# Kernel optimization log

Hardware: AMD Instinct MI355X
Metric: run time of the kernel (lower is better)

The kernel has to match this reference:

```python
import jax, jax.numpy as jnp
import numpy as np

NUM_NODES = 100000
NUM_EDGES = 2500000
NUM_GRAPHS = 512
NODE_DIM = 7
STATE_DIM = 32
M = 2
ROUNDS = 4


def setup_inputs() -> dict:
    key = jax.random.key(0)
    ks = jax.random.split(key, 16)
    x = jax.random.normal(ks[0], (NUM_NODES, NODE_DIM), dtype=jnp.float32)
    edge_index = jax.random.randint(ks[1], (2, NUM_EDGES), 0, NUM_NODES)
    batch = jnp.sort(jax.random.randint(ks[2], (NUM_NODES,), 0, NUM_GRAPHS))
    s = 1.0 / np.sqrt(STATE_DIM)
    W_in = jax.random.normal(ks[3], (NODE_DIM, STATE_DIM), dtype=jnp.float32) / np.sqrt(NODE_DIM)
    b_in = jnp.zeros((STATE_DIM,), dtype=jnp.float32)
    W_msg = jax.random.normal(ks[4], (ROUNDS, STATE_DIM, STATE_DIM), dtype=jnp.float32) * s
    b_msg = jnp.zeros((ROUNDS, STATE_DIM), dtype=jnp.float32)
    W_upd = jax.random.normal(ks[5], (ROUNDS, STATE_DIM, STATE_DIM), dtype=jnp.float32) * s
    b_upd = jnp.zeros((ROUNDS, STATE_DIM), dtype=jnp.float32)
    W_out = jax.random.normal(ks[6], (STATE_DIM, 2 * M), dtype=jnp.float32) * s
    b_out = jnp.zeros((2 * M,), dtype=jnp.float32)
    return {"x": x, "edge_index": edge_index, "batch": batch,
            "W_in": W_in, "b_in": b_in, "W_msg": W_msg, "b_msg": b_msg,
            "W_upd": W_upd, "b_upd": b_upd, "W_out": W_out, "b_out": b_out}


def reference(x, edge_index, batch, W_in, b_in, W_msg, b_msg, W_upd, b_upd, W_out, b_out):
    # input net
    state = jax.nn.relu(x @ W_in + b_in)  # (N, S)
    src, dst = edge_index[0], edge_index[1]
    for r in range(ROUNDS):
        message = jax.nn.relu(state @ W_msg[r] + b_msg[r])          # (N, S)
        gathered = message[src]                                      # (E, S) irregular gather
        aggregated = jax.ops.segment_sum(gathered, dst, num_segments=NUM_NODES)  # scatter-add
        state = state + jax.nn.relu(aggregated @ W_upd[r] + b_upd[r])
    graph_state = jax.ops.segment_sum(state, batch, num_segments=NUM_GRAPHS)     # (G, S)
    out = graph_state @ W_out + b_out                                # (G, 2M)
    mean, log_std = jnp.split(out, 2, axis=-1)
    # Gaussian head: return mean and std (scale = exp(log_std)) concatenated
    return jnp.concatenate([mean, jnp.exp(log_std)], axis=-1)
```

## Files before the change

### kernel.cpp

```cpp
#include <hip/hip_runtime.h>
#include <hip/hip_fp8.h>
#include <math.h>

#define N_NODES 100000
#define N_EDGES 2500000
#define N_GRAPHS 512
#define NODE_DIM 7
#define S 32
#define ROUNDS 4

#define BKT_SHIFT 7
#define BKT_NODES 128
#define NBKT ((N_NODES + BKT_NODES - 1) / BKT_NODES)
#define CAP 3712
#define NSLOT 64
#define SLOT_PAD 32

#define GN (N_NODES * S / 256)
#define GG (N_NODES / 16)

__device__ __forceinline__ void block_max_publish(float v, float* slots, int bid, int tid) {
    __shared__ float wmax[4];
#pragma unroll
    for (int o = 32; o > 0; o >>= 1) v = fmaxf(v, __shfl_xor(v, o, 64));
    if ((tid & 63) == 0) wmax[tid >> 6] = v;
    __syncthreads();
    if (tid == 0) {
        float m = fmaxf(fmaxf(wmax[0], wmax[1]), fmaxf(wmax[2], wmax[3]));
        atomicMax((unsigned int*)&slots[(bid & (NSLOT - 1)) * SLOT_PAD], __float_as_uint(m));
    }
}

__device__ __forceinline__ void acc4_fp8(unsigned int u, float& a0, float& a1,
                                         float& a2, float& a3) {
#if __has_builtin(__builtin_amdgcn_cvt_pk_f32_fp8)
    typedef float v2f __attribute__((ext_vector_type(2)));
    v2f lo = __builtin_amdgcn_cvt_pk_f32_fp8((int)u, false);
    v2f hi = __builtin_amdgcn_cvt_pk_f32_fp8((int)u, true);
    a0 += lo.x; a1 += lo.y; a2 += hi.x; a3 += hi.y;
#else
    __hip_fp8_e4m3 t0, t1, t2, t3;
    t0.__x = u & 0xff; t1.__x = (u >> 8) & 0xff;
    t2.__x = (u >> 16) & 0xff; t3.__x = (u >> 24) & 0xff;
    a0 += (float)t0; a1 += (float)t1; a2 += (float)t2; a3 += (float)t3;
#endif
}

__global__ void k_input(const float* __restrict__ x, const float* __restrict__ W_in,
                        const float* __restrict__ b_in, float* __restrict__ state,
                        float* __restrict__ graph_state, int* __restrict__ cursor,
                        float* __restrict__ tmpmax) {
    __shared__ float sW[NODE_DIM * S];
    __shared__ float sb[S];
    __shared__ float wmax[4];
    int tid = threadIdx.x;
    if (tid < NODE_DIM * S) sW[tid] = W_in[tid];
    if (tid < S) sb[tid] = b_in[tid];
    __syncthreads();
    int gid = blockIdx.x * blockDim.x + tid;
    if (gid < N_GRAPHS * S) graph_state[gid] = 0.f;
    if (gid < NBKT) cursor[gid] = 0;
    int n = gid >> 5, j = gid & 31;
    float acc = sb[j];
#pragma unroll
    for (int k = 0; k < NODE_DIM; k++) acc += x[n * NODE_DIM + k] * sW[k * S + j];
    float v = fmaxf(acc, 0.f);
    state[gid] = v;
#pragma unroll
    for (int o = 32; o > 0; o >>= 1) v = fmaxf(v, __shfl_xor(v, o, 64));
    if ((tid & 63) == 0) wmax[tid >> 6] = v;
    __syncthreads();
    if (tid == 0)
        tmpmax[blockIdx.x] = fmaxf(fmaxf(wmax[0], wmax[1]), fmaxf(wmax[2], wmax[3]));
}

__global__ void k_bin(const int* __restrict__ src, const int* __restrict__ dst,
                      int* __restrict__ cursor, int* __restrict__ binned,
                      const float* __restrict__ tmpmax, float* __restrict__ smax0) {
    __shared__ int cnt[NBKT];
    __shared__ int base[NBKT];
    __shared__ float red[16];
    int tid = threadIdx.x;
    if (blockIdx.x == 0) {
        float m = 0.f;
        for (int i = tid; i < GN; i += 1024) m = fmaxf(m, tmpmax[i]);
#pragma unroll
        for (int o = 32; o > 0; o >>= 1) m = fmaxf(m, __shfl_xor(m, o, 64));
        if ((tid & 63) == 0) red[tid >> 6] = m;
        __syncthreads();
        if (tid == 0) {
            float g = 0.f;
#pragma unroll
            for (int k = 0; k < 16; k++) g = fmaxf(g, red[k]);
            smax0[0] = g;
        } else if (tid < NSLOT) {
            smax0[tid * SLOT_PAD] = 0.f;
        }
    }
    int tile = (N_EDGES + gridDim.x - 1) / gridDim.x;
    int b0 = blockIdx.x * tile;
    int b1 = min(b0 + tile, N_EDGES);
    for (int i = tid; i < NBKT; i += blockDim.x) cnt[i] = 0;
    __syncthreads();
    int dv[10];
#pragma unroll
    for (int q = 0; q < 10; q++) {
        int e = b0 + tid + q * 1024;
        dv[q] = (e < b1) ? dst[e] : -1;
        if (dv[q] >= 0) atomicAdd(&cnt[dv[q] >> BKT_SHIFT], 1);
    }
    __syncthreads();
    for (int i = tid; i < NBKT; i += blockDim.x) {
        int c = cnt[i];
        base[i] = c ? atomicAdd(&cursor[i], c) : 0;
        cnt[i] = 0;
    }
    __syncthreads();
#pragma unroll
    for (int q = 0; q < 10; q++) {
        int e = b0 + tid + q * 1024;
        int d = dv[q];
        if (d >= 0) {
            int k = d >> BKT_SHIFT;
            int lpos = base[k] + atomicAdd(&cnt[k], 1);
            if (lpos < CAP)
                binned[(size_t)k * CAP + lpos] = (src[e] << BKT_SHIFT) | (d & (BKT_NODES - 1));
        }
    }
}

__global__ void k_fill2(const int* __restrict__ cursor, int* __restrict__ binned,
                        int* __restrict__ row_beg, int* __restrict__ row_end) {
    __shared__ int stage[CAP];
    __shared__ int cnt[BKT_NODES];
    __shared__ int sm[BKT_NODES];
    int tid = threadIdx.x;
    int bkt = blockIdx.x;
    int beg = bkt * CAP;
    int m = min(cursor[bkt], CAP);
    for (int i = tid; i < m; i += 256) stage[i] = binned[beg + i];
    if (tid < BKT_NODES) cnt[tid] = 0;
    __syncthreads();
    for (int i = tid; i < m; i += 256) atomicAdd(&cnt[stage[i] & (BKT_NODES - 1)], 1);
    __syncthreads();
    int v = 0;
    if (tid < BKT_NODES) { v = cnt[tid]; sm[tid] = v; }
    __syncthreads();
    for (int off = 1; off < BKT_NODES; off <<= 1) {
        int add = 0;
        if (tid < BKT_NODES && tid >= off) add = sm[tid - off];
        __syncthreads();
        if (tid < BKT_NODES) sm[tid] += add;
        __syncthreads();
    }
    if (tid < BKT_NODES) {
        int excl = sm[tid] - v;
        cnt[tid] = excl;
        int n = bkt * BKT_NODES + tid;
        if (n < N_NODES) { row_beg[n] = beg + excl; row_end[n] = beg + excl + v; }
    }
    __syncthreads();
    for (int i = tid; i < m; i += 256) {
        int ent = stage[i];
        int p = atomicAdd(&cnt[ent & (BKT_NODES - 1)], 1);
        binned[beg + p] = ent >> BKT_SHIFT;
    }
}

__global__ void k_msg(const float* __restrict__ state, const float* __restrict__ W,
                      const float* __restrict__ b, const float* __restrict__ smax_slots,
                      float* __restrict__ smax_next, float* __restrict__ inv_scale_out,
                      __hip_fp8_e4m3* __restrict__ message) {
    __shared__ float sW[S * S];
    __shared__ float sb[S];
    __shared__ float ssc[S];
    int tid = threadIdx.x;
    if (blockIdx.x < NSLOT && tid == 0) smax_next[blockIdx.x * SLOT_PAD] = 0.f;
    for (int i = tid; i < S * S; i += 256) sW[i] = W[i];
    if (tid < S) sb[tid] = b[tid];
    __syncthreads();
    if (tid < S) {
        float smax = 0.f;
#pragma unroll
        for (int k = 0; k < NSLOT; k++) smax = fmaxf(smax, smax_slots[k * SLOT_PAD]);
        float cs = 0.f;
#pragma unroll
        for (int k = 0; k < S; k++) cs += fabsf(sW[k * S + tid]);
        float bound = smax * cs + fabsf(sb[tid]) + 1e-20f;
        int e = (int)floorf(log2f(400.f / bound));
        e = max(-60, min(60, e));
        ssc[tid] = exp2f((float)e);
        if (blockIdx.x == 0) inv_scale_out[tid] = exp2f((float)-e);
    }
    __syncthreads();
    int gid = blockIdx.x * 256 + tid;
    int j = tid & 31;
    float my = state[gid];
    float acc = sb[j];
#pragma unroll
    for (int k = 0; k < S; k++) acc += __shfl(my, k, 32) * sW[k * S + j];
    float m = fminf(fmaxf(acc, 0.f) * ssc[j], 440.f);
    message[gid] = __hip_fp8_e4m3(m);
}

__global__ void k_gather_upd(const int* __restrict__ row_beg, const int* __restrict__ row_end,
                             const int* __restrict__ csr_src,
                             const unsigned char* __restrict__ message,
                             const float* __restrict__ W, const float* __restrict__ b,
                             const float* __restrict__ inv_scale,
                             float* __restrict__ state, float* __restrict__ smax_next) {
    __shared__ float sW[S * S];
    __shared__ float sb[S];
    __shared__ float si[S];
    int tid = threadIdx.x;
    for (int i = tid; i < S * S; i += 256) sW[i] = W[i];
    if (tid < S) { sb[tid] = b[tid]; si[tid] = inv_scale[tid]; }
    __syncthreads();
    int g = tid >> 5, j = tid & 31;
    int n0 = blockIdx.x * 16 + g * 2;
    int n1 = n0 + 1;
    int es = j >> 3;
    int qd = j & 7;
    int b0 = row_beg[n0], e0 = row_end[n0];
    int b1 = row_beg[n1], e1 = row_end[n1];
    float a0 = 0.f, a1 = 0.f, a2 = 0.f, a3 = 0.f;
    float c0 = 0.f, c1 = 0.f, c2 = 0.f, c3 = 0.f;
    int sid0 = (b0 + j < e0) ? csr_src[b0 + j] : 0;
    int sid1 = (b1 + j < e1) ? csr_src[b1 + j] : 0;
    while (b0 < e0 || b1 < e1) {
        unsigned int u0[8], u1[8];
#pragma unroll
        for (int p = 0; p < 8; p++) {
            int s = __shfl(sid0, p * 4 + es, 32);
            unsigned int* ap = (unsigned int*)(message + (unsigned)s * 32u + (unsigned)qd * 4u);
            u0[p] = __hip_atomic_load(ap, __ATOMIC_RELAXED, __HIP_MEMORY_SCOPE_AGENT);
        }
#pragma unroll
        for (int p = 0; p < 8; p++) {
            int s = __shfl(sid1, p * 4 + es, 32);
            unsigned int* ap = (unsigned int*)(message + (unsigned)s * 32u + (unsigned)qd * 4u);
            u1[p] = __hip_atomic_load(ap, __ATOMIC_RELAXED, __HIP_MEMORY_SCOPE_AGENT);
        }
        int nb0 = b0 + 32, nb1 = b1 + 32;
        int nsid0 = (nb0 + j < e0) ? csr_src[nb0 + j] : 0;
        int nsid1 = (nb1 + j < e1) ? csr_src[nb1 + j] : 0;
#pragma unroll
        for (int p = 0; p < 8; p++) {
            unsigned int uv = (b0 + p * 4 + es < e0) ? u0[p] : 0u;
            acc4_fp8(uv, a0, a1, a2, a3);
        }
#pragma unroll
        for (int p = 0; p < 8; p++) {
            unsigned int uv = (b1 + p * 4 + es < e1) ? u1[p] : 0u;
            acc4_fp8(uv, c0, c1, c2, c3);
        }
        b0 = nb0; b1 = nb1; sid0 = nsid0; sid1 = nsid1;
    }
    a0 += __shfl_xor(a0, 8, 32); a0 += __shfl_xor(a0, 16, 32);
    a1 += __shfl_xor(a1, 8, 32); a1 += __shfl_xor(a1, 16, 32);
    a2 += __shfl_xor(a2, 8, 32); a2 += __shfl_xor(a2, 16, 32);
    a3 += __shfl_xor(a3, 8, 32); a3 += __shfl_xor(a3, 16, 32);
    c0 += __shfl_xor(c0, 8, 32); c0 += __shfl_xor(c0, 16, 32);
    c1 += __shfl_xor(c1, 8, 32); c1 += __shfl_xor(c1, 16, 32);
    c2 += __shfl_xor(c2, 8, 32); c2 += __shfl_xor(c2, 16, 32);
    c3 += __shfl_xor(c3, 8, 32); c3 += __shfl_xor(c3, 16, 32);
    float s0 = si[4 * qd + 0], s1 = si[4 * qd + 1];
    float s2 = si[4 * qd + 2], s3 = si[4 * qd + 3];
    a0 *= s0; a1 *= s1; a2 *= s2; a3 *= s3;
    c0 *= s0; c1 *= s1; c2 *= s2; c3 *= s3;
    float u0v = sb[j], u1v = sb[j];
#pragma unroll
    for (int k = 0; k < S; k++) {
        float av, cv;
        switch (k & 3) {
            case 0: av = __shfl(a0, k >> 2, 32); cv = __shfl(c0, k >> 2, 32); break;
            case 1: av = __shfl(a1, k >> 2, 32); cv = __shfl(c1, k >> 2, 32); break;
            case 2: av = __shfl(a2, k >> 2, 32); cv = __shfl(c2, k >> 2, 32); break;
            default: av = __shfl(a3, k >> 2, 32); cv = __shfl(c3, k >> 2, 32); break;
        }
        float w = sW[k * S + j];
        u0v += av * w;
        u1v += cv * w;
    }
    size_t i0 = (size_t)n0 * S + j, i1 = (size_t)n1 * S + j;
    float ns0 = state[i0] + fmaxf(u0v, 0.f);
    float ns1 = state[i1] + fmaxf(u1v, 0.f);
    state[i0] = ns0;
    state[i1] = ns1;
    block_max_publish(fmaxf(ns0, ns1), smax_next, blockIdx.x, tid);
}

__global__ void k_pool(const float* __restrict__ state, const int* __restrict__ batch,
                       float* __restrict__ graph_state) {
    const int CHUNK = 32;
    const int nchunks = (N_NODES + CHUNK - 1) / CHUNK;
    int gid = blockIdx.x * blockDim.x + threadIdx.x;
    if (gid >= nchunks * S) return;
    int c = gid >> 5, j = gid & 31;
    int n0 = c * CHUNK;
    int n1 = min(n0 + CHUNK, N_NODES);
    float acc = 0.f;
    int curb = batch[n0];
    for (int n = n0; n < n1; n++) {
        int bn = batch[n];
        if (bn != curb) {
            atomicAdd(&graph_state[curb * S + j], acc);
            acc = 0.f;
            curb = bn;
        }
        acc += state[(size_t)n * S + j];
    }
    atomicAdd(&graph_state[curb * S + j], acc);
}

__global__ void k_head(const float* __restrict__ graph_state, const float* __restrict__ W_out,
                       const float* __restrict__ b_out, float* __restrict__ out) {
    int gid = blockIdx.x * blockDim.x + threadIdx.x;
    if (gid >= N_GRAPHS * 4) return;
    int g = gid >> 2, j = gid & 3;
    float acc = b_out[j];
#pragma unroll
    for (int k = 0; k < S; k++) acc += graph_state[g * S + k] * W_out[k * 4 + j];
    out[gid] = (j < 2) ? acc : expf(fminf(acc, 88.0f));
}

extern "C" void kernel_launch(void* const* d_in, const int* in_sizes, int n_in,
                              void* d_out, int out_size, void* d_ws, size_t ws_size,
                              hipStream_t stream) {
    const float* x     = (const float*)d_in[0];
    const int*   ei    = (const int*)d_in[1];
    const int*   batch = (const int*)d_in[2];
    const float* W_in  = (const float*)d_in[3];
    const float* b_in  = (const float*)d_in[4];
    const float* W_msg = (const float*)d_in[5];
    const float* b_msg = (const float*)d_in[6];
    const float* W_upd = (const float*)d_in[7];
    const float* b_upd = (const float*)d_in[8];
    const float* W_out = (const float*)d_in[9];
    const float* b_out = (const float*)d_in[10];
    float* out = (float*)d_out;

    float* state            = (float*)d_ws;
    __hip_fp8_e4m3* message = (__hip_fp8_e4m3*)(state + (size_t)N_NODES * S);
    float* graph_state      = (float*)((char*)message + (size_t)N_NODES * S);
    float* smax             = graph_state + N_GRAPHS * S;
    float* inv_scale        = smax + (ROUNDS + 1) * NSLOT * SLOT_PAD;
    float* tmpmax           = inv_scale + S;
    int*   row_beg          = (int*)(tmpmax + GN);
    int*   row_end          = row_beg + N_NODES;
    int*   cursor           = row_end + N_NODES;
    int*   binned           = cursor + NBKT;

    const int* src = ei;
    const int* dst = ei + N_EDGES;

    k_input<<<GN, dim3(256), 0, stream>>>(x, W_in, b_in, state, graph_state, cursor, tmpmax);
    k_bin<<<256, dim3(1024), 0, stream>>>(src, dst, cursor, binned, tmpmax, smax);
    k_fill2<<<NBKT, dim3(256), 0, stream>>>(cursor, binned, row_beg, row_end);

    for (int r = 0; r < ROUNDS; r++) {
        k_msg<<<GN, dim3(256), 0, stream>>>(state, W_msg + r * S * S, b_msg + r * S,
                                            smax + r * NSLOT * SLOT_PAD,
                                            smax + (r + 1) * NSLOT * SLOT_PAD,
                                            inv_scale, message);
        k_gather_upd<<<GG, dim3(256), 0, stream>>>(row_beg, row_end, binned,
                                                   (const unsigned char*)message,
                                                   W_upd + r * S * S, b_upd + r * S,
                                                   inv_scale, state,
                                                   smax + (r + 1) * NSLOT * SLOT_PAD);
    }

    const int CHUNK = 32;
    int nchunks = (N_NODES + CHUNK - 1) / CHUNK;
    int gP = (nchunks * S + 255) / 256;
    k_pool<<<gP, dim3(256), 0, stream>>>(state, batch, graph_state);

    k_head<<<(N_GRAPHS * 4 + 255) / 256, dim3(256), 0, stream>>>(graph_state, W_out, b_out, out);
}
```

Baseline: 369.9 us.

## Fuse CSR fill with first message kernel and enlarge dst buckets

Merges the bucket-local CSR fill and the round-0 message computation into one launch, where extra blocks beyond the bucket count run the message body, so one kernel launch goes away and the two independent jobs overlap. Buckets grow to 256 nodes with a larger capacity, which halves the bucket count and lets every thread of the 256-thread block own one node in the scan. The binning loop switches from a register-cached unrolled pass to a strided loop that reads dst twice. The gather kernel also drops software prefetching of the next csr_src chunk. Larger shared staging per block and the lost prefetch may cut occupancy and latency hiding.

```diff
diff --git a/kernel.cpp b/kernel.cpp
--- a/kernel.cpp
+++ b/kernel.cpp
@@ -9,10 +9,10 @@
 #define S 32
 #define ROUNDS 4
 
-#define BKT_SHIFT 7
-#define BKT_NODES 128
+#define BKT_SHIFT 8
+#define BKT_NODES 256
 #define NBKT ((N_NODES + BKT_NODES - 1) / BKT_NODES)
-#define CAP 3712
+#define CAP 7168
 #define NSLOT 64
 #define SLOT_PAD 32
 
@@ -46,6 +46,43 @@
 #endif
 }
 
+__device__ __forceinline__ void msg_body(int mb, int tid,
+                                         const float* __restrict__ state,
+                                         const float* __restrict__ W,
+                                         const float* __restrict__ b,
+                                         const float* __restrict__ smax_slots,
+                                         float* __restrict__ smax_next,
+                                         float* __restrict__ inv_scale_out,
+                                         __hip_fp8_e4m3* __restrict__ message,
+                                         float* sW, float* sb, float* ssc) {
+    if (mb < NSLOT && tid == 0) smax_next[mb * SLOT_PAD] = 0.f;
+    for (int i = tid; i < S * S; i += 256) sW[i] = W[i];
+    if (tid < S) sb[tid] = b[tid];
+    __syncthreads();
+    if (tid < S) {
+        float smax = 0.f;
+#pragma unroll
+        for (int k = 0; k < NSLOT; k++) smax = fmaxf(smax, smax_slots[k * SLOT_PAD]);
+        float cs = 0.f;
+#pragma unroll
+        for (int k = 0; k < S; k++) cs += fabsf(sW[k * S + tid]);
+        float bound = smax * cs + fabsf(sb[tid]) + 1e-20f;
+        int e = (int)floorf(log2f(400.f / bound));
+        e = max(-60, min(60, e));
+        ssc[tid] = exp2f((float)e);
+        if (mb == 0) inv_scale_out[tid] = exp2f((float)-e);
+    }
+    __syncthreads();
+    int gid = mb * 256 + tid;
+    int j = tid & 31;
+    float my = state[gid];
+    float acc = sb[j];
+#pragma unroll
+    for (int k = 0; k < S; k++) acc += __shfl(my, k, 32) * sW[k * S + j];
+    float m = fminf(fmaxf(acc, 0.f) * ssc[j], 440.f);
+    message[gid] = __hip_fp8_e4m3(m);
+}
+
 __global__ void k_input(const float* __restrict__ x, const float* __restrict__ W_in,
                         const float* __restrict__ b_in, float* __restrict__ state,
                         float* __restrict__ graph_state, int* __restrict__ cursor,
@@ -102,13 +139,8 @@
     int b1 = min(b0 + tile, N_EDGES);
     for (int i = tid; i < NBKT; i += blockDim.x) cnt[i] = 0;
     __syncthreads();
-    int dv[10];
-#pragma unroll
-    for (int q = 0; q < 10; q++) {
-        int e = b0 + tid + q * 1024;
-        dv[q] = (e < b1) ? dst[e] : -1;
-        if (dv[q] >= 0) atomicAdd(&cnt[dv[q] >> BKT_SHIFT], 1);
-    }
+    for (int e = b0 + tid; e < b1; e += blockDim.x)
+        atomicAdd(&cnt[dst[e] >> BKT_SHIFT], 1);
     __syncthreads();
     for (int i = tid; i < NBKT; i += blockDim.x) {
         int c = cnt[i];
@@ -116,53 +148,58 @@
         cnt[i] = 0;
     }
     __syncthreads();
-#pragma unroll
-    for (int q = 0; q < 10; q++) {
-        int e = b0 + tid + q * 1024;
-        int d = dv[q];
-        if (d >= 0) {
-            int k = d >> BKT_SHIFT;
-            int lpos = base[k] + atomicAdd(&cnt[k], 1);
-            if (lpos < CAP)
-                binned[(size_t)k * CAP + lpos] = (src[e] << BKT_SHIFT) | (d & (BKT_NODES - 1));
-        }
-    }
-}
-
-__global__ void k_fill2(const int* __restrict__ cursor, int* __restrict__ binned,
-                        int* __restrict__ row_beg, int* __restrict__ row_end) {
-    __shared__ int stage[CAP];
-    __shared__ int cnt[BKT_NODES];
-    __shared__ int sm[BKT_NODES];
+    for (int e = b0 + tid; e < b1; e += blockDim.x) {
+        int d = dst[e];
+        int k = d >> BKT_SHIFT;
+        int lpos = base[k] + atomicAdd(&cnt[k], 1);
+        if (lpos < CAP)
+            binned[(size_t)k * CAP + lpos] = (src[e] << BKT_SHIFT) | (d & (BKT_NODES - 1));
+    }
+}
+
+__global__ void k_fill_msg(const int* __restrict__ cursor, int* __restrict__ binned,
+                           int* __restrict__ row_beg, int* __restrict__ row_end,
+                           const float* __restrict__ state, const float* __restrict__ W,
+                           const float* __restrict__ b, const float* __restrict__ smax_slots,
+                           float* __restrict__ smax_next, float* __restrict__ inv_scale_out,
+                           __hip_fp8_e4m3* __restrict__ message) {
+    __shared__ union {
+        struct { int stage[CAP]; int cnt[BKT_NODES]; int sm[BKT_NODES]; } f;
+        struct { float sW[S * S]; float sb[S]; float ssc[S]; } m;
+    } u;
     int tid = threadIdx.x;
+    if (blockIdx.x >= NBKT) {
+        msg_body(blockIdx.x - NBKT, tid, state, W, b, smax_slots, smax_next,
+                 inv_scale_out, message, u.m.sW, u.m.sb, u.m.ssc);
+        return;
+    }
     int bkt = blockIdx.x;
     int beg = bkt * CAP;
     int m = min(cursor[bkt], CAP);
-    for (int i = tid; i < m; i += 256) stage[i] = binned[beg + i];
-    if (tid < BKT_NODES) cnt[tid] = 0;
-    __syncthreads();
-    for (int i = tid; i < m; i += 256) atomicAdd(&cnt[stage[i] & (BKT_NODES - 1)], 1);
-    __syncthreads();
-    int v = 0;
-    if (tid < BKT_NODES) { v = cnt[tid]; sm[tid] = v; }
+    for (int i = tid; i < m; i += 256) u.f.stage[i] = binned[beg + i];
+    u.f.cnt[tid] = 0;
+    __syncthreads();
+    for (int i = tid; i < m; i += 256) atomicAdd(&u.f.cnt[u.f.stage[i] & (BKT_NODES - 1)], 1);
+    __syncthreads();
+    int v = u.f.cnt[tid];
+    u.f.sm[tid] = v;
     __syncthreads();
     for (int off = 1; off < BKT_NODES; off <<= 1) {
-        int add = 0;
-        if (tid < BKT_NODES && tid >= off) add = sm[tid - off];
+        int add = (tid >= off) ? u.f.sm[tid - off] : 0;
         __syncthreads();
-        if (tid < BKT_NODES) sm[tid] += add;
+        u.f.sm[tid] += add;
         __syncthreads();
     }
-    if (tid < BKT_NODES) {
-        int excl = sm[tid] - v;
-        cnt[tid] = excl;
+    {
+        int excl = u.f.sm[tid] - v;
+        u.f.cnt[tid] = excl;
         int n = bkt * BKT_NODES + tid;
         if (n < N_NODES) { row_beg[n] = beg + excl; row_end[n] = beg + excl + v; }
     }
     __syncthreads();
     for (int i = tid; i < m; i += 256) {
-        int ent = stage[i];
-        int p = atomicAdd(&cnt[ent & (BKT_NODES - 1)], 1);
+        int ent = u.f.stage[i];
+        int p = atomicAdd(&u.f.cnt[ent & (BKT_NODES - 1)], 1);
         binned[beg + p] = ent >> BKT_SHIFT;
     }
 }
@@ -174,33 +211,8 @@
     __shared__ float sW[S * S];
     __shared__ float sb[S];
     __shared__ float ssc[S];
-    int tid = threadIdx.x;
-    if (blockIdx.x < NSLOT && tid == 0) smax_next[blockIdx.x * SLOT_PAD] = 0.f;
-    for (int i = tid; i < S * S; i += 256) sW[i] = W[i];
-    if (tid < S) sb[tid] = b[tid];
-    __syncthreads();
-    if (tid < S) {
-        float smax = 0.f;
-#pragma unroll
-        for (int k = 0; k < NSLOT; k++) smax = fmaxf(smax, smax_slots[k * SLOT_PAD]);
-        float cs = 0.f;
-#pragma unroll
-        for (int k = 0; k < S; k++) cs += fabsf(sW[k * S + tid]);
-        float bound = smax * cs + fabsf(sb[tid]) + 1e-20f;
-        int e = (int)floorf(log2f(400.f / bound));
-        e = max(-60, min(60, e));
-        ssc[tid] = exp2f((float)e);
-        if (blockIdx.x == 0) inv_scale_out[tid] = exp2f((float)-e);
-    }
-    __syncthreads();
-    int gid = blockIdx.x * 256 + tid;
-    int j = tid & 31;
-    float my = state[gid];
-    float acc = sb[j];
-#pragma unroll
-    for (int k = 0; k < S; k++) acc += __shfl(my, k, 32) * sW[k * S + j];
-    float m = fminf(fmaxf(acc, 0.f) * ssc[j], 440.f);
-    message[gid] = __hip_fp8_e4m3(m);
+    msg_body(blockIdx.x, threadIdx.x, state, W, b, smax_slots, smax_next,
+             inv_scale_out, message, sW, sb, ssc);
 }
 
 __global__ void k_gather_upd(const int* __restrict__ row_beg, const int* __restrict__ row_end,
@@ -225,9 +237,9 @@
     int b1 = row_beg[n1], e1 = row_end[n1];
     float a0 = 0.f, a1 = 0.f, a2 = 0.f, a3 = 0.f;
     float c0 = 0.f, c1 = 0.f, c2 = 0.f, c3 = 0.f;
-    int sid0 = (b0 + j < e0) ? csr_src[b0 + j] : 0;
-    int sid1 = (b1 + j < e1) ? csr_src[b1 + j] : 0;
-    while (b0 < e0 || b1 < e1) {
+    for (; b0 < e0 || b1 < e1; b0 += 32, b1 += 32) {
+        int sid0 = (b0 + j < e0) ? csr_src[b0 + j] : 0;
+        int sid1 = (b1 + j < e1) ? csr_src[b1 + j] : 0;
         unsigned int u0[8], u1[8];
 #pragma unroll
         for (int p = 0; p < 8; p++) {
@@ -241,9 +253,6 @@
             unsigned int* ap = (unsigned int*)(message + (unsigned)s * 32u + (unsigned)qd * 4u);
             u1[p] = __hip_atomic_load(ap, __ATOMIC_RELAXED, __HIP_MEMORY_SCOPE_AGENT);
         }
-        int nb0 = b0 + 32, nb1 = b1 + 32;
-        int nsid0 = (nb0 + j < e0) ? csr_src[nb0 + j] : 0;
-        int nsid1 = (nb1 + j < e1) ? csr_src[nb1 + j] : 0;
 #pragma unroll
         for (int p = 0; p < 8; p++) {
             unsigned int uv = (b0 + p * 4 + es < e0) ? u0[p] : 0u;
@@ -254,7 +263,6 @@
             unsigned int uv = (b1 + p * 4 + es < e1) ? u1[p] : 0u;
             acc4_fp8(uv, c0, c1, c2, c3);
         }
-        b0 = nb0; b1 = nb1; sid0 = nsid0; sid1 = nsid1;
     }
     a0 += __shfl_xor(a0, 8, 32); a0 += __shfl_xor(a0, 16, 32);
     a1 += __shfl_xor(a1, 8, 32); a1 += __shfl_xor(a1, 16, 32);
@@ -356,9 +364,16 @@
 
     k_input<<<GN, dim3(256), 0, stream>>>(x, W_in, b_in, state, graph_state, cursor, tmpmax);
     k_bin<<<256, dim3(1024), 0, stream>>>(src, dst, cursor, binned, tmpmax, smax);
-    k_fill2<<<NBKT, dim3(256), 0, stream>>>(cursor, binned, row_beg, row_end);
-
-    for (int r = 0; r < ROUNDS; r++) {
+    k_fill_msg<<<NBKT + GN, dim3(256), 0, stream>>>(cursor, binned, row_beg, row_end,
+                                                    state, W_msg, b_msg,
+                                                    smax, smax + NSLOT * SLOT_PAD,
+                                                    inv_scale, message);
+    k_gather_upd<<<GG, dim3(256), 0, stream>>>(row_beg, row_end, binned,
+                                               (const unsigned char*)message,
+                                               W_upd, b_upd, inv_scale, state,
+                                               smax + NSLOT * SLOT_PAD);
+
+    for (int r = 1; r < ROUNDS; r++) {
         k_msg<<<GN, dim3(256), 0, stream>>>(state, W_msg + r * S * S, b_msg + r * S,
                                             smax + r * NSLOT * SLOT_PAD,
                                             smax + (r + 1) * NSLOT * SLOT_PAD,
```

Measured after the change: 360.0 us. -2.7%, faster.
